# Performance work log

Hardware: AMD Instinct MI355X
Metric: run time of the kernel (lower is better)

Reference implementation:

```python
import jax, jax.numpy as jnp
import numpy as np

NUM_HEADS = 8
NUM_GROUPS = 32
EPS = 1e-5
RESCALE = 1.0


def setup_inputs() -> dict:
    key = jax.random.key(0)
    ks = jax.random.split(key, 7)
    b, c, h, w = 16, 512, 32, 32
    return {
        "x": jax.random.normal(ks[0], (b, c, h, w), jnp.float32),
        "norm_w": jax.random.normal(ks[1], (c,), jnp.float32),
        "norm_b": jax.random.normal(ks[2], (c,), jnp.float32),
        "qkv_w": jax.random.normal(ks[3], (3 * c, c), jnp.float32) * (c ** -0.5),
        "qkv_b": jax.random.normal(ks[4], (3 * c,), jnp.float32) * 0.02,
        "proj_w": jax.random.normal(ks[5], (c, c), jnp.float32) * (c ** -0.5),
        "proj_b": jax.random.normal(ks[6], (c,), jnp.float32) * 0.02,
    }


def _group_norm(x, w, b):
    # x: [B, C, L]
    B, C, L = x.shape
    g = x.reshape(B, NUM_GROUPS, (C // NUM_GROUPS) * L)
    mu = jnp.mean(g, axis=-1, keepdims=True)
    var = jnp.var(g, axis=-1, keepdims=True)
    g = (g - mu) * jax.lax.rsqrt(var + EPS)
    return g.reshape(B, C, L) * w[None, :, None] + b[None, :, None]


def reference(x, norm_w, norm_b, qkv_w, qkv_b, proj_w, proj_b):
    b, c, hh, ww = x.shape
    L = hh * ww
    H = NUM_HEADS
    ch = c // H  # head dim

    xr = x.reshape(b, c, L)
    hid = _group_norm(xr, norm_w, norm_b)

    # 1x1 conv1d == matmul over channel dim: [3c, c] @ [b, c, L]
    qkv = jnp.einsum('oc,bcl->bol', qkv_w, hid) + qkv_b[None, :, None]
    # torch: reshape(b*H, 3*ch, L).split(ch) -> per-head contiguous [q|k|v] blocks
    qkv = qkv.reshape(b, H, 3, ch, L)
    q, k, v = qkv[:, :, 0], qkv[:, :, 1], qkv[:, :, 2]  # [b, H, ch, L]

    scale = 1.0 / (ch ** 0.25)
    weight = jnp.einsum('bhct,bhcs->bhts', q * scale, k * scale)
    weight = jax.nn.softmax(weight.astype(jnp.float32), axis=-1).astype(weight.dtype)
    a = jnp.einsum('bhts,bhcs->bhct', weight, v)  # [b, H, ch, L]

    h = a.reshape(b, c, L)
    h = jnp.einsum('oc,bcl->bol', proj_w, h) + proj_b[None, :, None]
    h = h.reshape(b, c, hh, ww)
    return (x + h) / RESCALE
```

## Files before the change

kernel.cpp:

```cpp
#include <hip/hip_runtime.h>
#include <hip/hip_bf16.h>
#include <stdint.h>


using f32x4  = __attribute__((ext_vector_type(4))) float;
using bf16x8 = __attribute__((ext_vector_type(8))) __bf16;
using s8v    = __attribute__((ext_vector_type(8))) short;
using s4v    = __attribute__((ext_vector_type(4))) short;

__device__ __forceinline__ short f2bf(float f){
  union { float f; unsigned u; } c; c.f = f;
  unsigned r = (c.u + 0x7FFFu + ((c.u >> 16) & 1u)) >> 16;
  return (short)r;
}

__device__ __forceinline__ float exp2_fast(float x){
#if __has_builtin(__builtin_amdgcn_exp2f)
  return __builtin_amdgcn_exp2f(x);
#else
  return exp2f(x);
#endif
}

__device__ __forceinline__ void gl_lds16(const void* g, void* l){
  __builtin_amdgcn_global_load_lds((const __attribute__((address_space(1))) void*)g,
                                   (__attribute__((address_space(3))) void*)l, 16, 0, 0);
}

__global__ __launch_bounds__(256) void k_pre(const float* __restrict__ x,
                                             const float* __restrict__ w,
                                             const float* __restrict__ bia,
                                             short* __restrict__ hid,
                                             const float* __restrict__ qw,
                                             const float* __restrict__ pw,
                                             const float* __restrict__ qb,
                                             short* __restrict__ qwb,
                                             short* __restrict__ pwb,
                                             float* __restrict__ qbp){
  int bid = blockIdx.x;
  int tid = threadIdx.x;
  if (bid >= 512){
    int i = (bid - 512) * 256 + tid;
    if (i < 786432){
      int o = i >> 9, kk = i & 511;
      int h = o / 192, rem = o - h*192;
      int nr = (rem >> 6)*512 + h*64 + (rem & 63);
      qwb[nr*512 + kk] = f2bf(qw[i]);
    } else if (i < 1048576){
      int j = i - 786432;
      pwb[j] = f2bf(pw[j]);
    } else if (i < 1050112){
      int o = i - 1048576;
      int h = o / 192, rem = o - h*192;
      qbp[(rem >> 6)*512 + h*64 + (rem & 63)] = qb[o];
    }
    return;
  }
  int b = bid >> 5;
  int g = bid & 31;
  const float* xg = x + ((size_t)b*512 + g*16)*1024;
  int l0 = tid * 4;
  float v[16][4];
  float s1 = 0.f, s2 = 0.f;
  #pragma unroll
  for (int c = 0; c < 16; c++){
    f32x4 t = *(const f32x4*)(xg + c*1024 + l0);
    #pragma unroll
    for (int j = 0; j < 4; j++){ v[c][j] = t[j]; s1 += t[j]; s2 += t[j]*t[j]; }
  }
  #pragma unroll
  for (int m = 32; m; m >>= 1){ s1 += __shfl_xor(s1, m); s2 += __shfl_xor(s2, m); }
  __shared__ float r1[4], r2[4];
  int wv = tid >> 6, ln = tid & 63;
  if (ln == 0){ r1[wv] = s1; r2[wv] = s2; }
  __syncthreads();
  s1 = r1[0]+r1[1]+r1[2]+r1[3];
  s2 = r2[0]+r2[1]+r2[2]+r2[3];
  float mu = s1 * (1.f/16384.f);
  float var = s2 * (1.f/16384.f) - mu*mu;
  float rs = rsqrtf(var + 1e-5f);
  float ww[16], bb[16];
  #pragma unroll
  for (int c = 0; c < 16; c++){ ww[c] = w[g*16+c]*rs; bb[c] = bia[g*16+c]; }
  #pragma unroll
  for (int j = 0; j < 4; j++){
    short o[16];
    #pragma unroll
    for (int c = 0; c < 16; c++) o[c] = f2bf((v[c][j]-mu)*ww[c] + bb[c]);
    short* dst = hid + ((size_t)(b*1024 + l0 + j))*512 + g*16;
    *(s8v*)dst     = *(s8v*)o;
    *(s8v*)(dst+8) = *(s8v*)(o+8);
  }
}

__global__ __launch_bounds__(256) void k_gemmQ(
    const short* __restrict__ A, const short* __restrict__ Bm,
    const float* __restrict__ bias,
    short* __restrict__ q_t, short* __restrict__ k_t, short* __restrict__ v_t)
{
  __shared__ short Lds[24576];
  int id = blockIdx.x;
  int xcd = id & 7, ix = id >> 3;
  int mt = ix % 6, nt = ix / 6;
  int m0 = mt * 256;
  int n0 = (xcd + 8*nt) * 128;
  int tid = threadIdx.x;
  int lane = tid & 63;
  int wv = tid >> 6;
  int wr = wv >> 1, wc = wv & 1;
  int l15 = lane & 15, g = lane >> 4;
  f32x4 acc[8][4] = {};

  auto STAGE = [&](int db, int t){
    int k0 = t * 32;
    #pragma unroll
    for (int i = 0; i < 6; i++){
      int cc = wv*6 + i;
      int row, byteoff;
      const short* srcb;
      if (cc < 16){ row = cc*16 + (lane>>2); srcb = A + (size_t)(m0+row)*512; byteoff = cc*1024; }
      else        { row = (cc-16)*16 + (lane>>2); srcb = Bm + (size_t)(n0+row)*512; byteoff = 16384 + (cc-16)*1024; }
      int slot = lane & 3;
      gl_lds16(srcb + k0 + ((slot ^ ((row>>1)&3))*8),
               (char*)Lds + db*24576 + byteoff);
    }
  };

  auto COMPUTE = [&](int db){
    const char* Ab = (const char*)Lds + db*24576;
    const char* Bb = Ab + 16384;
    bf16x8 af[8], bf[4];
    #pragma unroll
    for (int m = 0; m < 8; m++){
      int row = wr*128 + m*16 + l15;
      af[m] = *(const bf16x8*)(Ab + row*64 + ((g*16) ^ (((row>>1)&3)<<4)));
    }
    #pragma unroll
    for (int n = 0; n < 4; n++){
      int row = wc*64 + n*16 + l15;
      bf[n] = *(const bf16x8*)(Bb + row*64 + ((g*16) ^ (((row>>1)&3)<<4)));
    }
    __builtin_amdgcn_s_setprio(1);
    #pragma unroll
    for (int m = 0; m < 8; m++)
      #pragma unroll
      for (int n = 0; n < 4; n++)
        acc[m][n] = __builtin_amdgcn_mfma_f32_16x16x32_bf16(af[m], bf[n], acc[m][n], 0, 0, 0);
    __builtin_amdgcn_s_setprio(0);
  };

  STAGE(0, 0);
  for (int t = 0; t < 16; t++){
    __syncthreads();
    if (t < 15) STAGE((t+1)&1, t+1);
    COMPUTE(t&1);
  }

  int sel = m0 >> 9;
  if (sel < 2){
    const float sc = (sel == 0) ? 0.18033688011112042f : 1.0f;
    short* dstb = (sel == 0) ? q_t : k_t;
    #pragma unroll
    for (int m = 0; m < 8; m++){
      int ob = m0 + wr*128 + m*16 + (g<<2);
      int hh = (ob>>6)&7, c0 = ob&63;
      float bs[4];
      #pragma unroll
      for (int r = 0; r < 4; r++) bs[r] = bias[ob+r];
      #pragma unroll
      for (int n = 0; n < 4; n++){
        int nn = n0 + wc*64 + n*16 + l15;
        int bb = nn >> 10, ll = nn & 1023;
        int bh = bb*8 + hh;
        short o4[4];
        #pragma unroll
        for (int r = 0; r < 4; r++) o4[r] = f2bf((acc[m][n][r] + bs[r]) * sc);
        *(s4v*)(dstb + ((size_t)bh*1024 + ll)*64 + c0) = *(s4v*)o4;
      }
    }
  } else {
    short* Sc = Lds;
    int b0  = n0 >> 10;
    int s64 = (n0 >> 6) & 15;
    int hb  = (m0 - 1024) >> 6;
    #pragma unroll
    for (int ph = 0; ph < 2; ph++){
      __syncthreads();
      if (wr == ph){
        #pragma unroll
        for (int m = 0; m < 8; m++){
          int ob = m0 + wr*128 + m*16 + (g<<2);
          int h2 = (ob>>6)&1, cq = (ob>>4)&3;
          float bs[4];
          #pragma unroll
          for (int r = 0; r < 4; r++) bs[r] = bias[ob+r];
          #pragma unroll
          for (int n = 0; n < 4; n++){
            int nn = n0 + wc*64 + n*16 + l15;
            int sl = nn & 63, sreg = (nn>>6)&1;
            int ks2 = sl >> 5, gq = (sl>>2)&3, i2 = (sl&3) + 4*((sl>>4)&1);
            int base = (h2*2 + sreg)*4096 + (((ks2*4+gq)*4 + cq)*16 + (g<<2))*8 + i2;
            #pragma unroll
            for (int r = 0; r < 4; r++)
              Sc[base + r*8] = f2bf(acc[m][n][r] + bs[r]);
          }
        }
      }
      __syncthreads();
      #pragma unroll
      for (int it = 0; it < 8; it++){
        int flat = it*2048 + tid*8;
        int reg = flat >> 12, off = flat & 4095;
        int h2 = reg >> 1, sreg = reg & 1;
        int bh = b0*8 + hb + ph*2 + h2;
        *(s8v*)(v_t + ((size_t)bh*16 + s64 + sreg)*4096 + off) = *(const s8v*)(Sc + flat);
      }
    }
  }
}

__global__ __launch_bounds__(256) void k_gemmP(
    const short* __restrict__ A, const short* __restrict__ Bm,
    const float* __restrict__ bias, const float* __restrict__ xres,
    float* __restrict__ outp)
{
  __shared__ short Al[2][128*64];
  __shared__ short Bl[2][128*64];
  int id = blockIdx.x;
  int xcd = id & 7, ix = id >> 3;
  int mt = ix & 3, nt = ix >> 2;
  int m0 = mt * 128;
  int n0 = (xcd + 8*nt) * 128;
  int tid = threadIdx.x;
  int lane = tid & 63;
  int wv = tid >> 6;
  int wr = wv >> 1, wc = wv & 1;
  int l15 = lane & 15, g = lane >> 4;
  f32x4 acc[4][4] = {};

  auto STAGE = [&](int db, int t){
    int k0 = t * 64;
    #pragma unroll
    for (int i = 0; i < 8; i++){
      int cc = wv*8 + i;
      if (cc < 16){
        int slot = cc*64 + lane;
        int row = slot >> 3, off = slot & 7;
        gl_lds16(A + (size_t)(m0+row)*512 + k0 + (off ^ (row&7))*8,
                 (char*)Al[db] + cc*1024);
      } else {
        int slot = (cc-16)*64 + lane;
        int row = slot >> 3, off = slot & 7;
        gl_lds16(Bm + (size_t)(n0+row)*512 + k0 + (off ^ (row&7))*8,
                 (char*)Bl[db] + (cc-16)*1024);
      }
    }
  };

  auto COMPUTE = [&](int db){
    #pragma unroll
    for (int kk = 0; kk < 2; kk++){
      bf16x8 af[4], bf[4];
      #pragma unroll
      for (int m = 0; m < 4; m++){
        int row = wr*64 + m*16 + l15;
        int byte = row*128 + (((kk*64) + (g*16)) ^ ((row&7)<<4));
        af[m] = *(const bf16x8*)((char*)Al[db] + byte);
      }
      #pragma unroll
      for (int n = 0; n < 4; n++){
        int row = wc*64 + n*16 + l15;
        int byte = row*128 + (((kk*64) + (g*16)) ^ ((row&7)<<4));
        bf[n] = *(const bf16x8*)((char*)Bl[db] + byte);
      }
      __builtin_amdgcn_s_setprio(1);
      #pragma unroll
      for (int m = 0; m < 4; m++)
        #pragma unroll
        for (int n = 0; n < 4; n++)
          acc[m][n] = __builtin_amdgcn_mfma_f32_16x16x32_bf16(af[m], bf[n], acc[m][n], 0, 0, 0);
      __builtin_amdgcn_s_setprio(0);
    }
  };

  STAGE(0, 0);
  for (int t = 0; t < 8; t++){
    __syncthreads();
    if (t < 7) STAGE((t+1)&1, t+1);
    COMPUTE(t&1);
  }

  #pragma unroll
  for (int m = 0; m < 4; m++){
    int ob = m0 + wr*64 + m*16 + (g<<2);
    float bs[4];
    #pragma unroll
    for (int r = 0; r < 4; r++) bs[r] = bias[ob+r];
    #pragma unroll
    for (int n = 0; n < 4; n++){
      int nn = n0 + wc*64 + n*16 + l15;
      int bb = nn >> 10, ll = nn & 1023;
      #pragma unroll
      for (int r = 0; r < 4; r++){
        size_t idx = ((size_t)bb*512 + ob + r)*1024 + ll;
        outp[idx] = xres[idx] + acc[m][n][r] + bs[r];
      }
    }
  }
}

__global__ __launch_bounds__(256, 4) void k_attn(
    const short* __restrict__ q_t, const short* __restrict__ k_t,
    const short* __restrict__ v_t, short* __restrict__ a_bt)
{
  __shared__ short Kh[4*2048];
  __shared__ short Vh[4*2048];
  int id = blockIdx.x;
  int xcd = id & 7, ix = id >> 3;
  int bh = xcd*16 + (ix >> 3);
  int qb = ix & 7;
  int bb = bh >> 3, hh = bh & 7;
  int tid = threadIdx.x;
  int lane = tid & 63;
  int wv = tid >> 6;
  int l15 = lane & 15, g = lane >> 4;

  bf16x8 qf[2][2];
  #pragma unroll
  for (int qt = 0; qt < 2; qt++){
    const short* qbase = q_t + ((size_t)bh*1024 + qb*128 + qt*64 + wv*16 + l15)*64 + g*8;
    qf[qt][0] = *(const bf16x8*)(qbase);
    qf[qt][1] = *(const bf16x8*)(qbase + 32);
  }
  asm volatile("" :: "v"(qf[0][0]), "v"(qf[0][1]), "v"(qf[1][0]), "v"(qf[1][1]));

  bf16x8 onesb;
  #pragma unroll
  for (int i = 0; i < 8; i++) onesb[i] = (__bf16)1.0f;

  f32x4 o[2][4] = {};
  f32x4 osum[2] = {};

  auto STAGE = [&](int db, int h){
    int t64 = h >> 1, ks = h & 1;
    #pragma unroll
    for (int i = 0; i < 2; i++){
      int cc = wv*2 + i;
      if (cc < 4){
        int row = cc*8 + (lane>>3), slot = lane & 7;
        gl_lds16(k_t + ((size_t)bh*1024 + h*32 + row)*64 + ((slot ^ (row&7))*8),
                 (char*)Kh + db*4096 + cc*1024);
      } else {
        gl_lds16(v_t + ((size_t)bh*16 + t64)*4096 + ks*2048 + (cc-4)*512 + lane*8,
                 (char*)Vh + db*4096 + (cc-4)*1024);
      }
    }
  };

  auto COMPUTE = [&](int db){
    const char* Kb = (const char*)Kh + db*4096;
    const char* Vb = (const char*)Vh + db*4096;
    f32x4 scl[2][2] = {};
    #pragma unroll
    for (int jl = 0; jl < 2; jl++){
      int row = jl*16 + l15;
      int swz = (row&7)<<4;
      bf16x8 kf0 = *(const bf16x8*)(Kb + row*128 + ((g*16) ^ swz));
      bf16x8 kf1 = *(const bf16x8*)(Kb + row*128 + ((64 + g*16) ^ swz));
      __builtin_amdgcn_s_setprio(1);
      #pragma unroll
      for (int qt = 0; qt < 2; qt++){
        scl[qt][jl] = __builtin_amdgcn_mfma_f32_16x16x32_bf16(kf0, qf[qt][0], scl[qt][jl], 0, 0, 0);
        scl[qt][jl] = __builtin_amdgcn_mfma_f32_16x16x32_bf16(kf1, qf[qt][1], scl[qt][jl], 0, 0, 0);
      }
      __builtin_amdgcn_s_setprio(0);
    }
    bf16x8 pa[2];
    #pragma unroll
    for (int qt = 0; qt < 2; qt++){
      #pragma unroll
      for (int i2 = 0; i2 < 8; i2++)
        pa[qt][i2] = (__bf16)exp2_fast(scl[qt][i2>>2][i2&3]);
      osum[qt] = __builtin_amdgcn_mfma_f32_16x16x32_bf16(pa[qt], onesb, osum[qt], 0, 0, 0);
    }
    #pragma unroll
    for (int jd = 0; jd < 4; jd++){
      bf16x8 vbb = *(const bf16x8*)(Vb + (g*4+jd)*256 + l15*16);
      __builtin_amdgcn_s_setprio(1);
      #pragma unroll
      for (int qt = 0; qt < 2; qt++)
        o[qt][jd] = __builtin_amdgcn_mfma_f32_16x16x32_bf16(pa[qt], vbb, o[qt][jd], 0, 0, 0);
      __builtin_amdgcn_s_setprio(0);
    }
  };

  STAGE(0, 0);
  STAGE(1, 1);
  #pragma unroll 2
  for (int h = 0; h < 30; h++){
    STAGE((h+2)&3, h+2);
    asm volatile("s_waitcnt vmcnt(4)" ::: "memory");
    __builtin_amdgcn_s_barrier();
    __builtin_amdgcn_sched_barrier(0);
    COMPUTE(h&3);
  }
  asm volatile("s_waitcnt vmcnt(2)" ::: "memory");
  __builtin_amdgcn_s_barrier();
  __builtin_amdgcn_sched_barrier(0);
  COMPUTE(2);
  asm volatile("s_waitcnt vmcnt(0)" ::: "memory");
  __builtin_amdgcn_s_barrier();
  __builtin_amdgcn_sched_barrier(0);
  COMPUTE(3);

  #pragma unroll
  for (int qt = 0; qt < 2; qt++){
    #pragma unroll
    for (int r = 0; r < 4; r++){
      float inv = 1.f / osum[qt][r];
      int qrow = qb*128 + qt*64 + wv*16 + g*4 + r;
      #pragma unroll
      for (int jd = 0; jd < 4; jd++)
        a_bt[((size_t)bb*1024 + qrow)*512 + hh*64 + jd*16 + l15] = f2bf(o[qt][jd][r] * inv);
    }
  }
}

extern "C" void kernel_launch(void* const* d_in, const int* in_sizes, int n_in,
                              void* d_out, int out_size, void* d_ws, size_t ws_size,
                              hipStream_t stream){
  const float* x  = (const float*)d_in[0];
  const float* nw = (const float*)d_in[1];
  const float* nb = (const float*)d_in[2];
  const float* qw = (const float*)d_in[3];
  const float* qb = (const float*)d_in[4];
  const float* pw = (const float*)d_in[5];
  const float* pb = (const float*)d_in[6];
  float* outp = (float*)d_out;

  char* ws = (char*)d_ws;
  short* hid  = (short*)(ws);
  short* qwb  = (short*)(ws + 16777216);
  short* pwb  = (short*)(ws + 18350080);
  short* q_t  = (short*)(ws + 18874368);
  short* k_t  = (short*)(ws + 35651584);
  short* v_t  = (short*)(ws + 52428800);
  short* a_bt = hid;
  float* qbp  = (float*)d_out;
  if (ws_size < 69206016) return;

  k_pre<<<4615, 256, 0, stream>>>(x, nw, nb, hid, qw, pw, qb, qwb, pwb, qbp);
  k_gemmQ<<<768, 256, 0, stream>>>(qwb, hid, qbp, q_t, k_t, v_t);
  k_attn<<<1024, 256, 0, stream>>>(q_t, k_t, v_t, a_bt);
  k_gemmP<<<512, 256, 0, stream>>>(pwb, a_bt, pb, x, outp);
}
```

Baseline: 136.2 us.

## Retile QKV GEMM to 128x128x64 and double per-block query rows in attention

The QKV GEMM drops from 256x128 tiles with K-step 32 to 128x128 tiles with K-step 64. It doubles the grid, adds a new XOR swizzle, and runs a single-phase V-transpose epilogue through LDS. The attention kernel now processes 256 query rows per block instead of 128, halving the grid and reusing each staged K/V tile across twice as many queries. To fit the extra register pressure it lowers the occupancy hint from 4 to 2 and removes the unroll. The aim is to cut K/V staging traffic and barrier overhead per query, at the cost of fewer resident waves for latency hiding.

```diff
diff --git a/kernel.cpp b/kernel.cpp
--- a/kernel.cpp
+++ b/kernel.cpp
@@ -98,71 +98,80 @@
     const float* __restrict__ bias,
     short* __restrict__ q_t, short* __restrict__ k_t, short* __restrict__ v_t)
 {
-  __shared__ short Lds[24576];
+  __shared__ short Al[2][128*64];
+  __shared__ short Bl[2][128*64];
   int id = blockIdx.x;
   int xcd = id & 7, ix = id >> 3;
-  int mt = ix % 6, nt = ix / 6;
-  int m0 = mt * 256;
+  int mt = ix % 12, nt = ix / 12;
+  int m0 = mt * 128;
   int n0 = (xcd + 8*nt) * 128;
   int tid = threadIdx.x;
   int lane = tid & 63;
   int wv = tid >> 6;
   int wr = wv >> 1, wc = wv & 1;
   int l15 = lane & 15, g = lane >> 4;
-  f32x4 acc[8][4] = {};
+  f32x4 acc[4][4] = {};
 
   auto STAGE = [&](int db, int t){
-    int k0 = t * 32;
-    #pragma unroll
-    for (int i = 0; i < 6; i++){
-      int cc = wv*6 + i;
-      int row, byteoff;
-      const short* srcb;
-      if (cc < 16){ row = cc*16 + (lane>>2); srcb = A + (size_t)(m0+row)*512; byteoff = cc*1024; }
-      else        { row = (cc-16)*16 + (lane>>2); srcb = Bm + (size_t)(n0+row)*512; byteoff = 16384 + (cc-16)*1024; }
-      int slot = lane & 3;
-      gl_lds16(srcb + k0 + ((slot ^ ((row>>1)&3))*8),
-               (char*)Lds + db*24576 + byteoff);
+    int k0 = t * 64;
+    #pragma unroll
+    for (int i = 0; i < 8; i++){
+      int cc = wv*8 + i;
+      if (cc < 16){
+        int slot = cc*64 + lane;
+        int row = slot >> 3, off = slot & 7;
+        gl_lds16(A + (size_t)(m0+row)*512 + k0 + (off ^ (row&7))*8,
+                 (char*)Al[db] + cc*1024);
+      } else {
+        int slot = (cc-16)*64 + lane;
+        int row = slot >> 3, off = slot & 7;
+        gl_lds16(Bm + (size_t)(n0+row)*512 + k0 + (off ^ (row&7))*8,
+                 (char*)Bl[db] + (cc-16)*1024);
+      }
     }
   };
 
   auto COMPUTE = [&](int db){
-    const char* Ab = (const char*)Lds + db*24576;
-    const char* Bb = Ab + 16384;
-    bf16x8 af[8], bf[4];
-    #pragma unroll
-    for (int m = 0; m < 8; m++){
-      int row = wr*128 + m*16 + l15;
-      af[m] = *(const bf16x8*)(Ab + row*64 + ((g*16) ^ (((row>>1)&3)<<4)));
-    }
-    #pragma unroll
-    for (int n = 0; n < 4; n++){
-      int row = wc*64 + n*16 + l15;
-      bf[n] = *(const bf16x8*)(Bb + row*64 + ((g*16) ^ (((row>>1)&3)<<4)));
-    }
-    __builtin_amdgcn_s_setprio(1);
-    #pragma unroll
-    for (int m = 0; m < 8; m++)
-      #pragma unroll
-      for (int n = 0; n < 4; n++)
-        acc[m][n] = __builtin_amdgcn_mfma_f32_16x16x32_bf16(af[m], bf[n], acc[m][n], 0, 0, 0);
-    __builtin_amdgcn_s_setprio(0);
+    #pragma unroll
+    for (int kk = 0; kk < 2; kk++){
+      bf16x8 af[4], bf[4];
+      #pragma unroll
+      for (int m = 0; m < 4; m++){
+        int row = wr*64 + m*16 + l15;
+        int byte = row*128 + (((kk*64) + (g*16)) ^ ((row&7)<<4));
+        af[m] = *(const bf16x8*)((char*)Al[db] + byte);
+      }
+      #pragma unroll
+      for (int n = 0; n < 4; n++){
+        int row = wc*64 + n*16 + l15;
+        int byte = row*128 + (((kk*64) + (g*16)) ^ ((row&7)<<4));
+        bf[n] = *(const bf16x8*)((char*)Bl[db] + byte);
+      }
+      __builtin_amdgcn_s_setprio(1);
+      #pragma unroll
+      for (int m = 0; m < 4; m++)
+        #pragma unroll
+        for (int n = 0; n < 4; n++)
+          acc[m][n] = __builtin_amdgcn_mfma_f32_16x16x32_bf16(af[m], bf[n], acc[m][n], 0, 0, 0);
+      __builtin_amdgcn_s_setprio(0);
+    }
   };
 
   STAGE(0, 0);
-  for (int t = 0; t < 16; t++){
+  for (int t = 0; t < 8; t++){
     __syncthreads();
-    if (t < 15) STAGE((t+1)&1, t+1);
+    if (t < 7) STAGE((t+1)&1, t+1);
     COMPUTE(t&1);
   }
+  __syncthreads();
 
   int sel = m0 >> 9;
   if (sel < 2){
     const float sc = (sel == 0) ? 0.18033688011112042f : 1.0f;
     short* dstb = (sel == 0) ? q_t : k_t;
     #pragma unroll
-    for (int m = 0; m < 8; m++){
-      int ob = m0 + wr*128 + m*16 + (g<<2);
+    for (int m = 0; m < 4; m++){
+      int ob = m0 + wr*64 + m*16 + (g<<2);
       int hh = (ob>>6)&7, c0 = ob&63;
       float bs[4];
       #pragma unroll
@@ -179,42 +188,35 @@
       }
     }
   } else {
-    short* Sc = Lds;
+    short* Sc = (short*)Al;
+    #pragma unroll
+    for (int m = 0; m < 4; m++){
+      int ob = m0 + wr*64 + m*16 + (g<<2);
+      int h2 = (ob>>6)&1, cq = (ob>>4)&3;
+      float bs[4];
+      #pragma unroll
+      for (int r = 0; r < 4; r++) bs[r] = bias[ob+r];
+      #pragma unroll
+      for (int n = 0; n < 4; n++){
+        int nn = n0 + wc*64 + n*16 + l15;
+        int sl = nn & 63, sreg = (nn>>6)&1;
+        int ks2 = sl >> 5, gq = (sl>>2)&3, i2 = (sl&3) + 4*((sl>>4)&1);
+        int base = (h2*2 + sreg)*4096 + (((ks2*4+gq)*4 + cq)*16 + (g<<2))*8 + i2;
+        #pragma unroll
+        for (int r = 0; r < 4; r++)
+          Sc[base + r*8] = f2bf(acc[m][n][r] + bs[r]);
+      }
+    }
+    __syncthreads();
     int b0  = n0 >> 10;
     int s64 = (n0 >> 6) & 15;
     int hb  = (m0 - 1024) >> 6;
     #pragma unroll
-    for (int ph = 0; ph < 2; ph++){
-      __syncthreads();
-      if (wr == ph){
-        #pragma unroll
-        for (int m = 0; m < 8; m++){
-          int ob = m0 + wr*128 + m*16 + (g<<2);
-          int h2 = (ob>>6)&1, cq = (ob>>4)&3;
-          float bs[4];
-          #pragma unroll
-          for (int r = 0; r < 4; r++) bs[r] = bias[ob+r];
-          #pragma unroll
-          for (int n = 0; n < 4; n++){
-            int nn = n0 + wc*64 + n*16 + l15;
-            int sl = nn & 63, sreg = (nn>>6)&1;
-            int ks2 = sl >> 5, gq = (sl>>2)&3, i2 = (sl&3) + 4*((sl>>4)&1);
-            int base = (h2*2 + sreg)*4096 + (((ks2*4+gq)*4 + cq)*16 + (g<<2))*8 + i2;
-            #pragma unroll
-            for (int r = 0; r < 4; r++)
-              Sc[base + r*8] = f2bf(acc[m][n][r] + bs[r]);
-          }
-        }
-      }
-      __syncthreads();
-      #pragma unroll
-      for (int it = 0; it < 8; it++){
-        int flat = it*2048 + tid*8;
-        int reg = flat >> 12, off = flat & 4095;
-        int h2 = reg >> 1, sreg = reg & 1;
-        int bh = b0*8 + hb + ph*2 + h2;
-        *(s8v*)(v_t + ((size_t)bh*16 + s64 + sreg)*4096 + off) = *(const s8v*)(Sc + flat);
-      }
+    for (int it = 0; it < 8; it++){
+      int flat = it*2048 + tid*8;
+      int h2 = flat >> 13, rem = flat & 8191, sreg = rem >> 12, off = rem & 4095;
+      int bh = b0*8 + hb + h2;
+      *(s8v*)(v_t + ((size_t)bh*16 + s64 + sreg)*4096 + off) = *(const s8v*)(Sc + flat);
     }
   }
 }
@@ -309,7 +311,7 @@
   }
 }
 
-__global__ __launch_bounds__(256, 4) void k_attn(
+__global__ __launch_bounds__(256, 2) void k_attn(
     const short* __restrict__ q_t, const short* __restrict__ k_t,
     const short* __restrict__ v_t, short* __restrict__ a_bt)
 {
@@ -317,29 +319,30 @@
   __shared__ short Vh[4*2048];
   int id = blockIdx.x;
   int xcd = id & 7, ix = id >> 3;
-  int bh = xcd*16 + (ix >> 3);
-  int qb = ix & 7;
+  int bh = xcd*16 + (ix >> 2);
+  int qb = ix & 3;
   int bb = bh >> 3, hh = bh & 7;
   int tid = threadIdx.x;
   int lane = tid & 63;
   int wv = tid >> 6;
   int l15 = lane & 15, g = lane >> 4;
 
-  bf16x8 qf[2][2];
-  #pragma unroll
-  for (int qt = 0; qt < 2; qt++){
-    const short* qbase = q_t + ((size_t)bh*1024 + qb*128 + qt*64 + wv*16 + l15)*64 + g*8;
+  bf16x8 qf[4][2];
+  #pragma unroll
+  for (int qt = 0; qt < 4; qt++){
+    const short* qbase = q_t + ((size_t)bh*1024 + qb*256 + qt*64 + wv*16 + l15)*64 + g*8;
     qf[qt][0] = *(const bf16x8*)(qbase);
     qf[qt][1] = *(const bf16x8*)(qbase + 32);
   }
-  asm volatile("" :: "v"(qf[0][0]), "v"(qf[0][1]), "v"(qf[1][0]), "v"(qf[1][1]));
+  asm volatile("" :: "v"(qf[0][0]), "v"(qf[0][1]), "v"(qf[1][0]), "v"(qf[1][1]),
+                     "v"(qf[2][0]), "v"(qf[2][1]), "v"(qf[3][0]), "v"(qf[3][1]));
 
   bf16x8 onesb;
   #pragma unroll
   for (int i = 0; i < 8; i++) onesb[i] = (__bf16)1.0f;
 
-  f32x4 o[2][4] = {};
-  f32x4 osum[2] = {};
+  f32x4 o[4][4] = {};
+  f32x4 osum[4] = {};
 
   auto STAGE = [&](int db, int h){
     int t64 = h >> 1, ks = h & 1;
@@ -360,7 +363,7 @@
   auto COMPUTE = [&](int db){
     const char* Kb = (const char*)Kh + db*4096;
     const char* Vb = (const char*)Vh + db*4096;
-    f32x4 scl[2][2] = {};
+    f32x4 scl[4][2] = {};
     #pragma unroll
     for (int jl = 0; jl < 2; jl++){
       int row = jl*16 + l15;
@@ -369,15 +372,15 @@
       bf16x8 kf1 = *(const bf16x8*)(Kb + row*128 + ((64 + g*16) ^ swz));
       __builtin_amdgcn_s_setprio(1);
       #pragma unroll
-      for (int qt = 0; qt < 2; qt++){
+      for (int qt = 0; qt < 4; qt++){
         scl[qt][jl] = __builtin_amdgcn_mfma_f32_16x16x32_bf16(kf0, qf[qt][0], scl[qt][jl], 0, 0, 0);
         scl[qt][jl] = __builtin_amdgcn_mfma_f32_16x16x32_bf16(kf1, qf[qt][1], scl[qt][jl], 0, 0, 0);
       }
       __builtin_amdgcn_s_setprio(0);
     }
-    bf16x8 pa[2];
-    #pragma unroll
-    for (int qt = 0; qt < 2; qt++){
+    bf16x8 pa[4];
+    #pragma unroll
+    for (int qt = 0; qt < 4; qt++){
       #pragma unroll
       for (int i2 = 0; i2 < 8; i2++)
         pa[qt][i2] = (__bf16)exp2_fast(scl[qt][i2>>2][i2&3]);
@@ -388,7 +391,7 @@
       bf16x8 vbb = *(const bf16x8*)(Vb + (g*4+jd)*256 + l15*16);
       __builtin_amdgcn_s_setprio(1);
       #pragma unroll
-      for (int qt = 0; qt < 2; qt++)
+      for (int qt = 0; qt < 4; qt++)
         o[qt][jd] = __builtin_amdgcn_mfma_f32_16x16x32_bf16(pa[qt], vbb, o[qt][jd], 0, 0, 0);
       __builtin_amdgcn_s_setprio(0);
     }
@@ -396,7 +399,6 @@
 
   STAGE(0, 0);
   STAGE(1, 1);
-  #pragma unroll 2
   for (int h = 0; h < 30; h++){
     STAGE((h+2)&3, h+2);
     asm volatile("s_waitcnt vmcnt(4)" ::: "memory");
@@ -414,11 +416,11 @@
   COMPUTE(3);
 
   #pragma unroll
-  for (int qt = 0; qt < 2; qt++){
+  for (int qt = 0; qt < 4; qt++){
     #pragma unroll
     for (int r = 0; r < 4; r++){
       float inv = 1.f / osum[qt][r];
-      int qrow = qb*128 + qt*64 + wv*16 + g*4 + r;
+      int qrow = qb*256 + qt*64 + wv*16 + g*4 + r;
       #pragma unroll
       for (int jd = 0; jd < 4; jd++)
         a_bt[((size_t)bb*1024 + qrow)*512 + hh*64 + jd*16 + l15] = f2bf(o[qt][jd][r] * inv);
@@ -450,7 +452,7 @@
   if (ws_size < 69206016) return;
 
   k_pre<<<4615, 256, 0, stream>>>(x, nw, nb, hid, qw, pw, qb, qwb, pwb, qbp);
-  k_gemmQ<<<768, 256, 0, stream>>>(qwb, hid, qbp, q_t, k_t, v_t);
-  k_attn<<<1024, 256, 0, stream>>>(q_t, k_t, v_t, a_bt);
+  k_gemmQ<<<1536, 256, 0, stream>>>(qwb, hid, qbp, q_t, k_t, v_t);
+  k_attn<<<512, 256, 0, stream>>>(q_t, k_t, v_t, a_bt);
   k_gemmP<<<512, 256, 0, stream>>>(pwb, a_bt, pb, x, outp);
 }
```

Measured after the change: 119.6 us. 1.14x faster.
